# Optimization experiments

Measured on AMD Instinct MI355X. Metric: run time of the kernel, lower is better.

## Reference

```python
import jax, jax.numpy as jnp
import numpy as np

TAU = 0.5

def setup_inputs() -> dict:
    key = jax.random.key(0)
    ks = jax.random.split(key, 20)
    B, D1, D2, E1, E2, U = 4096, 2000, 2000, 256, 256, 512
    M = E1 + E2
    s = lambda k, shp, scale=0.05: jax.random.normal(k, shp, dtype=jnp.float32) * scale
    return {
        "inputs": jax.random.normal(ks[0], (B, D1 + D2), dtype=jnp.float32),
        "h_tm1": jax.random.normal(ks[1], (B, U), dtype=jnp.float32),
        "crohis_tm": jax.random.normal(ks[2], (B, M), dtype=jnp.float32),
        "embed_weight_1": s(ks[3], (D1, E1)),
        "embed_weight_2": s(ks[4], (D2, E2)),
        "ca_1to2_w": s(ks[5], (E1, E1)),
        "ca_1to2_u": s(ks[6], (E2, E1)),
        "ca_1to2_v": s(ks[7], (E2, E1)),
        "ca_2to1_w": s(ks[8], (E2, E2)),
        "ca_2to1_u": s(ks[9], (E1, E2)),
        "ca_2to1_v": s(ks[10], (E1, E2)),
        "crohis_weight_w": s(ks[11], (M, U)),
        "crohis_bias": jnp.zeros((U,), jnp.float32),
        "crohis_decomp_weight": s(ks[12], (M, M)),
        "crohis_decomp_bias": jnp.zeros((M,), jnp.float32),
        "kernel": s(ks[13], (M, 3 * U)),
        "recurrent_kernel": s(ks[14], (U, 3 * U)),
        "bias": jnp.zeros((3 * U,), jnp.float32),
    }


def reference(inputs, h_tm1, crohis_tm,
              embed_weight_1, embed_weight_2,
              ca_1to2_w, ca_1to2_u, ca_1to2_v,
              ca_2to1_w, ca_2to1_u, ca_2to1_v,
              crohis_weight_w, crohis_bias,
              crohis_decomp_weight, crohis_decomp_bias,
              kernel, recurrent_kernel, bias):
    D1 = embed_weight_1.shape[0]
    U = recurrent_kernel.shape[0]
    # dual embedding lookups (dense multi-hot x embedding matrix)
    seqx1 = inputs[:, :D1]
    seqx2 = inputs[:, D1:]
    emb1 = seqx1 @ embed_weight_1   # [B, E1]
    emb2 = seqx2 @ embed_weight_2   # [B, E2]
    # cross-attention gates (softmax over feature axis, as K.softmax default)
    att12 = jax.nn.softmax(jnp.tanh(emb1 @ ca_1to2_w + emb2 @ ca_1to2_u) * (emb2 @ ca_1to2_v), axis=-1)
    att21 = jax.nn.softmax(jnp.tanh(emb2 @ ca_2to1_w + emb1 @ ca_2to1_u) * (emb1 @ ca_2to1_v), axis=-1)
    x = jnp.concatenate([emb1 * att12, emb2 * att21], axis=-1)  # [B, M]
    # cross-history decomposition modulating previous hidden state
    cro = jnp.tanh(crohis_tm @ crohis_decomp_weight + crohis_decomp_bias)
    h_prev = h_tm1 + jnp.tanh(cro @ crohis_weight_w + crohis_bias)
    # GRU (implementation=2, reset_after=False)
    mx = x @ kernel + bias                         # [B, 3U]
    x_z, x_r, x_h = mx[:, :U], mx[:, U:2 * U], mx[:, 2 * U:]
    mi = h_prev @ recurrent_kernel[:, :2 * U]      # [B, 2U]
    z = jax.nn.sigmoid(x_z + mi[:, :U])
    r = jax.nn.sigmoid(x_r + mi[:, U:])
    hh = jnp.tanh(x_h + (r * h_prev) @ recurrent_kernel[:, 2 * U:])
    h = z * h_prev + (1.0 - z) * hh
    # updated cross-history state (exponential moving average with tau)
    crohis_new = TAU * crohis_tm + (1.0 - TAU) * x
    return h, crohis_new
```

## Files before the change

### kernel.cpp

```cpp
#include <hip/hip_runtime.h>
#include <hip/hip_bf16.h>
#include <math.h>


#define TAU_F 0.5f

typedef __bf16 bf16x8 __attribute__((ext_vector_type(8)));
typedef __bf16 bf16x4 __attribute__((ext_vector_type(4)));
typedef float f32x4 __attribute__((ext_vector_type(4)));

__device__ __forceinline__ void gload16(const void* g, void* l) {
    __builtin_amdgcn_global_load_lds(
        (const __attribute__((address_space(1))) void*)g,
        (__attribute__((address_space(3))) void*)l, 16, 0, 0);
}

struct SubGemm {
    const void* A;
    int lda;
    int Kvalid;
    const __bf16* BT;
    int ldbt;
    float* C;
    int ldc;
    long long strideC;
    int Ksub;
    int nbx;
    int pairSplit;
    int pairAOff;
};

template <bool AFP32>
__global__ __launch_bounds__(256) void gemm_dual(SubGemm g1, SubGemm g2, int blocks1)
{
    __shared__ __bf16 As[4][64][32];
    __shared__ __bf16 Bs[4][128][32];

    const int tid = threadIdx.x, w = tid >> 6, l = tid & 63;

    const int gx = gridDim.x;
    const int nwg = gx * (int)gridDim.y;
    const int hw = (int)blockIdx.y * gx + (int)blockIdx.x;
    const int lg = (hw & 7) * (nwg >> 3) + (hw >> 3);
    const int bxl_lin = lg % gx;
    const int by = lg / gx;

    const bool second = bxl_lin >= blocks1;
    const SubGemm& g = second ? g2 : g1;
    const int bxl = second ? bxl_lin - blocks1 : bxl_lin;
    const int ct = bxl % g.nbx, spl = bxl / g.nbx;
    const int brow = by * 64, bcol = ct * 128;
    const int k_begin = spl * g.Ksub;
    const int nt = g.Ksub >> 5;
    float* C = g.C + (size_t)spl * g.strideC;
    const int aoff = (ct >= g.pairSplit) ? g.pairAOff : 0;

    const int sar = w * 16 + (l >> 2);
    const int sbr = w * 32 + (l >> 2);
    const int seg = (l & 3) * 8;

    const __bf16* Ab  = (const __bf16*)g.A + aoff + (size_t)(brow + sar) * g.lda + seg + k_begin;
    const float*  Af  = (const float*)g.A + aoff + (size_t)(brow + sar) * g.lda;
    const __bf16* Bg0 = g.BT + (size_t)(bcol + sbr) * g.ldbt + seg + k_begin;
    const __bf16* Bg1 = Bg0 + (size_t)16 * g.ldbt;
    const int kcl = g.Kvalid - 8;

    f32x4 acc[2][4] = {};
    const int fr = l & 15, fk = (l >> 4) * 8;
    const int wr = (w >> 1) * 32, wc = (w & 1) * 64;
    const int kmax = (nt - 1) * 32;

#define ISSUE_B(slot)                                                      \
    {                                                                      \
        const int _s = (slot);                                             \
        const int _k = (_s * 32 < kmax) ? _s * 32 : kmax;                  \
        const int _b = _s & 3;                                             \
        gload16(Bg0 + _k, &Bs[_b][w * 32][0]);                             \
        gload16(Bg1 + _k, &Bs[_b][w * 32 + 16][0]);                        \
    }
#define ISSUE_AB(slot)                                                     \
    {                                                                      \
        const int _s = (slot);                                             \
        const int _k = (_s * 32 < kmax) ? _s * 32 : kmax;                  \
        const int _b = _s & 3;                                             \
        gload16(Ab + _k,  &As[_b][w * 16][0]);                             \
        gload16(Bg0 + _k, &Bs[_b][w * 32][0]);                             \
        gload16(Bg1 + _k, &Bs[_b][w * 32 + 16][0]);                        \
    }

    if constexpr (AFP32) {
        f32x4 r0a, r0b, r1a, r1b, r2a, r2b, r3a, r3b;

        auto aload = [&](int slot, f32x4& ra, f32x4& rb) {
            int c = k_begin + slot * 32 + seg;
            c = c < kcl ? c : kcl;
            ra = *(const f32x4*)(Af + c);
            rb = *(const f32x4*)(Af + c + 4);
        };
        auto awrite = [&](int bufi, f32x4& ra, f32x4& rb) {
            __bf16 o[8];
#pragma unroll
            for (int z = 0; z < 4; ++z) { o[z] = (__bf16)ra[z]; o[4 + z] = (__bf16)rb[z]; }
            *(bf16x8*)&As[bufi][sar][seg] = *(bf16x8*)o;
        };
        auto astep = [&](int t, f32x4& wa, f32x4& wb, f32x4& la, f32x4& lb) {
            asm volatile("s_waitcnt vmcnt(4)" ::: "memory");
            asm volatile("s_waitcnt lgkmcnt(0)" ::: "memory");
            __builtin_amdgcn_s_barrier();
            const int bi = t & 3;
            bf16x8 a[2], b[4];
#pragma unroll
            for (int m = 0; m < 2; ++m) a[m] = *(const bf16x8*)&As[bi][wr + m * 16 + fr][fk];
#pragma unroll
            for (int n = 0; n < 4; ++n) b[n] = *(const bf16x8*)&Bs[bi][wc + n * 16 + fr][fk];
            awrite((t + 1) & 3, wa, wb);
            aload(t + 3, la, lb);
            ISSUE_B(t + 2)
#pragma unroll
            for (int m = 0; m < 2; ++m)
#pragma unroll
                for (int n = 0; n < 4; ++n)
                    acc[m][n] = __builtin_amdgcn_mfma_f32_16x16x32_bf16(a[m], b[n], acc[m][n], 0, 0, 0);
        };

        aload(0, r0a, r0b);
        asm volatile("s_waitcnt vmcnt(0)" ::: "memory");
        awrite(0, r0a, r0b);
        aload(1, r1a, r1b);
        ISSUE_B(0)
        aload(2, r2a, r2b);
        ISSUE_B(1)

        for (int t = 0; t < nt; t += 4) {
            astep(t,     r1a, r1b, r3a, r3b);
            astep(t + 1, r2a, r2b, r0a, r0b);
            astep(t + 2, r3a, r3b, r1a, r1b);
            astep(t + 3, r0a, r0b, r2a, r2b);
        }
    } else {
        ISSUE_AB(0) ISSUE_AB(1) ISSUE_AB(2)
        for (int t = 0; t < nt; ++t) {
            asm volatile("s_waitcnt vmcnt(6)" ::: "memory");
            asm volatile("s_waitcnt lgkmcnt(0)" ::: "memory");
            __builtin_amdgcn_s_barrier();
            const int bi = t & 3;
            bf16x8 a[2], b[4];
#pragma unroll
            for (int m = 0; m < 2; ++m) a[m] = *(const bf16x8*)&As[bi][wr + m * 16 + fr][fk];
#pragma unroll
            for (int n = 0; n < 4; ++n) b[n] = *(const bf16x8*)&Bs[bi][wc + n * 16 + fr][fk];
            ISSUE_AB(t + 3)
#pragma unroll
            for (int m = 0; m < 2; ++m)
#pragma unroll
                for (int n = 0; n < 4; ++n)
                    acc[m][n] = __builtin_amdgcn_mfma_f32_16x16x32_bf16(a[m], b[n], acc[m][n], 0, 0, 0);
        }
    }
#undef ISSUE_B
#undef ISSUE_AB

    const int fq = (l >> 4) * 4;
#pragma unroll
    for (int m = 0; m < 2; ++m)
#pragma unroll
        for (int n = 0; n < 4; ++n)
#pragma unroll
            for (int r = 0; r < 4; ++r) {
                int row = brow + wr + m * 16 + fq + r;
                int col = bcol + wc + n * 16 + fr;
                C[(size_t)row * g.ldc + col] = acc[m][n][r];
            }
}

__global__ __launch_bounds__(256) void prep_wT(
    const float* __restrict__ ew1, const float* __restrict__ ew2,
    const float* __restrict__ w12, const float* __restrict__ u12,
    const float* __restrict__ v12, const float* __restrict__ w21,
    const float* __restrict__ u21, const float* __restrict__ v21,
    const float* __restrict__ cd_w, const float* __restrict__ cw_w,
    const float* __restrict__ kern, const float* __restrict__ rkern,
    __bf16* __restrict__ WT, __bf16* __restrict__ WcatT,
    __bf16* __restrict__ cdT, __bf16* __restrict__ cwT,
    __bf16* __restrict__ kernT, __bf16* __restrict__ rkernT)
{
    __shared__ float tile[64][65];
    const int b = blockIdx.x, tid = threadIdx.x;
    const int tr = tid >> 6, tc = tid & 63;

    const float* src = nullptr;
    int ldsrc = 0, srow0 = 0, scol0 = 0, kvalid = 1 << 30;
    __bf16* dst; int ldd, n0, k0;
    bool zero = false;

    if (b < 256) {
        int q = b; n0 = (q >> 5) * 64; k0 = (q & 31) * 64;
        dst = WT; ldd = 2048; kvalid = 2000; ldsrc = 256; srow0 = k0;
        if (n0 < 256) { src = ew1; scol0 = n0; } else { src = ew2; scol0 = n0 - 256; }
    } else if (b < 384) {
        int q = b - 256; n0 = (q >> 3) * 64; k0 = (q & 7) * 64;
        dst = WcatT; ldd = 512; ldsrc = 256; srow0 = k0 & 255; scol0 = n0 & 255;
        int qn = n0 >> 8; bool khi = k0 >= 256;
        if (qn == 0)      src = khi ? u12 : w12;
        else if (qn == 1) src = khi ? w21 : u21;
        else if (qn == 2) { if (khi) src = v12; else zero = true; }
        else              { if (khi) zero = true; else src = v21; }
    } else if (b < 448) {
        int q = b - 384; n0 = (q >> 3) * 64; k0 = (q & 7) * 64;
        src = cd_w; ldsrc = 512; srow0 = k0; scol0 = n0; dst = cdT; ldd = 512;
    } else if (b < 512) {
        int q = b - 448; n0 = (q >> 3) * 64; k0 = (q & 7) * 64;
        src = cw_w; ldsrc = 512; srow0 = k0; scol0 = n0; dst = cwT; ldd = 512;
    } else if (b < 704) {
        int q = b - 512; n0 = (q >> 3) * 64; k0 = (q & 7) * 64;
        src = kern; ldsrc = 1536; srow0 = k0; scol0 = n0; dst = kernT; ldd = 512;
    } else {
        int q = b - 704; n0 = (q >> 3) * 64; k0 = (q & 7) * 64;
        src = rkern; ldsrc = 1536; srow0 = k0; scol0 = n0; dst = rkernT; ldd = 512;
    }

#pragma unroll
    for (int p = 0; p < 16; ++p) {
        int kr = p * 4 + tr;
        float v = 0.f;
        if (!zero && (srow0 + kr) < kvalid)
            v = src[(size_t)(srow0 + kr) * ldsrc + scol0 + tc];
        tile[kr][tc] = v;
    }
    __syncthreads();
#pragma unroll
    for (int p = 0; p < 16; ++p) {
        int nr = p * 4 + tr;
        dst[(size_t)(n0 + nr) * ldd + k0 + tc] = (__bf16)tile[tc][nr];
    }
}

__global__ __launch_bounds__(256) void reduce_A(
    const float* __restrict__ P12, const float* __restrict__ P4,
    const float* __restrict__ cd_b,
    __bf16* __restrict__ E, __bf16* __restrict__ cro)
{
    int b = blockIdx.x;
    int i = (((b & 2047) * 256) + threadIdx.x) * 4;
    if (b < 2048) {
        f32x4 p0 = *(const f32x4*)(P12 + i);
        f32x4 p1 = *(const f32x4*)(P12 + (1 << 21) + i);
        __bf16 o[4];
#pragma unroll
        for (int j = 0; j < 4; ++j) o[j] = (__bf16)(p0[j] + p1[j]);
        *(bf16x4*)&E[i] = *(bf16x4*)o;
    } else {
        f32x4 p0 = *(const f32x4*)(P4 + i);
        int c = i & 511;
        __bf16 o[4];
#pragma unroll
        for (int j = 0; j < 4; ++j) o[j] = (__bf16)tanhf(p0[j] + cd_b[c + j]);
        *(bf16x4*)&cro[i] = *(bf16x4*)o;
    }
}

__global__ __launch_bounds__(256) void fuse1(
    const float* __restrict__ T, const __bf16* __restrict__ E,
    const float* __restrict__ crohis,
    const float* __restrict__ P5,
    const float* __restrict__ h_tm1, const float* __restrict__ cw_b,
    __bf16* __restrict__ x, float* __restrict__ cro_out,
    float* __restrict__ hprev, __bf16* __restrict__ hprev_bf)
{
    __shared__ float s4[4];
    int b = blockIdx.x;
    int j = threadIdx.x;
    if (b < 4096) {
        const float* t = T + (size_t)b * 1024;
        float s12 = tanhf(t[j])       * t[512 + j];
        float s21 = tanhf(t[256 + j]) * t[768 + j];
        float v = s12;
#pragma unroll
        for (int o = 32; o >= 1; o >>= 1) v = fmaxf(v, __shfl_xor(v, o, 64));
        __syncthreads(); if ((j & 63) == 0) s4[j >> 6] = v; __syncthreads();
        float m12 = fmaxf(fmaxf(s4[0], s4[1]), fmaxf(s4[2], s4[3]));
        float e12 = expf(s12 - m12);
        v = e12;
#pragma unroll
        for (int o = 32; o >= 1; o >>= 1) v += __shfl_xor(v, o, 64);
        __syncthreads(); if ((j & 63) == 0) s4[j >> 6] = v; __syncthreads();
        float sum12 = s4[0] + s4[1] + s4[2] + s4[3];
        v = s21;
#pragma unroll
        for (int o = 32; o >= 1; o >>= 1) v = fmaxf(v, __shfl_xor(v, o, 64));
        __syncthreads(); if ((j & 63) == 0) s4[j >> 6] = v; __syncthreads();
        float m21 = fmaxf(fmaxf(s4[0], s4[1]), fmaxf(s4[2], s4[3]));
        float e21 = expf(s21 - m21);
        v = e21;
#pragma unroll
        for (int o = 32; o >= 1; o >>= 1) v += __shfl_xor(v, o, 64);
        __syncthreads(); if ((j & 63) == 0) s4[j >> 6] = v; __syncthreads();
        float sum21 = s4[0] + s4[1] + s4[2] + s4[3];

        size_t b0 = (size_t)b * 512 + j, b1 = b0 + 256;
        float x1 = (float)E[b0] * (e12 / sum12);
        float x2 = (float)E[b1] * (e21 / sum21);
        x[b0] = (__bf16)x1;
        x[b1] = (__bf16)x2;
        cro_out[b0] = TAU_F * crohis[b0] + (1.f - TAU_F) * x1;
        cro_out[b1] = TAU_F * crohis[b1] + (1.f - TAU_F) * x2;
    } else {
        int i = ((b - 4096) * 256 + j) * 4;
        f32x4 p = *(const f32x4*)(P5 + i);
        f32x4 ht = *(const f32x4*)(h_tm1 + i);
        int c = i & 511;
        f32x4 o; __bf16 ob[4];
#pragma unroll
        for (int q = 0; q < 4; ++q) {
            float hv = ht[q] + tanhf(p[q] + cw_b[c + q]);
            o[q] = hv; ob[q] = (__bf16)hv;
        }
        *(f32x4*)(hprev + i) = o;
        *(bf16x4*)&hprev_bf[i] = *(bf16x4*)ob;
    }
}

__global__ __launch_bounds__(256) void gates_k(
    const float* __restrict__ mx, const float* __restrict__ mi2,
    const float* __restrict__ hprev, const float* __restrict__ bias,
    __bf16* __restrict__ rh)
{
    int i = (blockIdx.x * 256 + threadIdx.x) * 4;
    int row = i >> 9, c = i & 511;
    f32x4 a  = *(const f32x4*)(mx + (size_t)row * 1536 + 512 + c);
    f32x4 m  = *(const f32x4*)(mi2 + (size_t)row * 1024 + 512 + c);
    f32x4 hp = *(const f32x4*)(hprev + i);
    f32x4 bb = *(const f32x4*)(bias + 512 + c);
    __bf16 o[4];
#pragma unroll
    for (int q = 0; q < 4; ++q) {
        float r = 1.f / (1.f + expf(-(a[q] + bb[q] + m[q])));
        o[q] = (__bf16)(r * hp[q]);
    }
    *(bf16x4*)&rh[i] = *(bf16x4*)o;
}

__global__ __launch_bounds__(256) void final_k(
    const float* __restrict__ mx, const float* __restrict__ mi2,
    const float* __restrict__ P8a, const float* __restrict__ P8b,
    const float* __restrict__ hprev, const float* __restrict__ bias,
    float* __restrict__ h)
{
    int i = (blockIdx.x * 256 + threadIdx.x) * 4;
    int row = i >> 9, c = i & 511;
    f32x4 xz = *(const f32x4*)(mx + (size_t)row * 1536 + c);
    f32x4 xh = *(const f32x4*)(mx + (size_t)row * 1536 + 1024 + c);
    f32x4 mz = *(const f32x4*)(mi2 + (size_t)row * 1024 + c);
    f32x4 p0 = *(const f32x4*)(P8a + i);
    f32x4 p1 = *(const f32x4*)(P8b + i);
    f32x4 hp = *(const f32x4*)(hprev + i);
    f32x4 bz = *(const f32x4*)(bias + c);
    f32x4 bh = *(const f32x4*)(bias + 1024 + c);
    f32x4 o;
#pragma unroll
    for (int q = 0; q < 4; ++q) {
        float z = 1.f / (1.f + expf(-(xz[q] + bz[q] + mz[q])));
        float hh = tanhf(xh[q] + bh[q] + p0[q] + p1[q]);
        o[q] = z * hp[q] + (1.f - z) * hh;
    }
    *(f32x4*)(h + i) = o;
}

extern "C" void kernel_launch(void* const* d_in, const int* in_sizes, int n_in,
                              void* d_out, int out_size, void* d_ws, size_t ws_size,
                              hipStream_t stream)
{
    (void)in_sizes; (void)n_in; (void)out_size; (void)ws_size;

    const float* inputs = (const float*)d_in[0];
    const float* h_tm1  = (const float*)d_in[1];
    const float* crohis = (const float*)d_in[2];
    const float* ew1    = (const float*)d_in[3];
    const float* ew2    = (const float*)d_in[4];
    const float* ca12w  = (const float*)d_in[5];
    const float* ca12u  = (const float*)d_in[6];
    const float* ca12v  = (const float*)d_in[7];
    const float* ca21w  = (const float*)d_in[8];
    const float* ca21u  = (const float*)d_in[9];
    const float* ca21v  = (const float*)d_in[10];
    const float* cw_w   = (const float*)d_in[11];
    const float* cw_b   = (const float*)d_in[12];
    const float* cd_w   = (const float*)d_in[13];
    const float* cd_b   = (const float*)d_in[14];
    const float* kern   = (const float*)d_in[15];
    const float* rkern  = (const float*)d_in[16];
    const float* bias   = (const float*)d_in[17];

    char* ws = (char*)d_ws;
    const size_t MB = 1 << 20;
    float*  P12      = (float*)(ws + 0);
    float*  P4       = (float*)(ws + 16 * MB);
    __bf16* E        = (__bf16*)(ws + 32 * MB);
    __bf16* cro_bf   = (__bf16*)(ws + 36 * MB);
    float*  T        = (float*)(ws + 0);
    float*  P5       = (float*)(ws + 16 * MB);
    __bf16* x        = (__bf16*)(ws + 40 * MB);
    float*  hprev    = (float*)(ws + 24 * MB);
    __bf16* hprev_bf = (__bf16*)(ws + 64 * MB);
    float*  mx       = (float*)(ws + 0);
    float*  mi2      = (float*)(ws + 44 * MB);
    __bf16* rh       = (__bf16*)(ws + 32 * MB);
    float*  P8       = (float*)(ws + 36 * MB);
    float*  P8b      = (float*)(ws + 60 * MB);
    __bf16* WT       = (__bf16*)(ws + 68 * MB);
    __bf16* WcatT    = (__bf16*)(ws + 70 * MB);
    __bf16* cdT      = (__bf16*)(ws + 71 * MB);
    __bf16* cwT      = (__bf16*)(ws + 71 * MB + 512 * 1024);
    __bf16* kernT    = (__bf16*)(ws + 72 * MB);
    __bf16* rkernT   = (__bf16*)(ws + 73 * MB + 512 * 1024);

    float* h_out   = (float*)d_out;
    float* cro_out = (float*)d_out + 2 * 1048576;

    const int BIG = 1 << 30;

    prep_wT<<<896, 256, 0, stream>>>(ew1, ew2, ca12w, ca12u, ca12v, ca21w,
                                     ca21u, ca21v, cd_w, cw_w, kern, rkern,
                                     WT, WcatT, cdT, cwT, kernT, rkernT);

    SubGemm gA1 = { inputs, 4000, 2000, WT,  2048, P12, 512, 1ll << 21, 1024, 4, 2, 2000 };
    SubGemm gA2 = { crohis,  512,  512, cdT,  512, P4,  512, 0,          512, 4, BIG, 0 };
    gemm_dual<true><<<dim3(12, 64), 256, 0, stream>>>(gA1, gA2, 8);

    reduce_A<<<4096, 256, 0, stream>>>(P12, P4, cd_b, E, cro_bf);

    SubGemm gB1 = { E,      512, 512, WcatT, 512, T,  1024, 0, 512, 8, BIG, 0 };
    SubGemm gB2 = { cro_bf, 512, 512, cwT,   512, P5, 512,  0, 512, 4, BIG, 0 };
    gemm_dual<false><<<dim3(12, 64), 256, 0, stream>>>(gB1, gB2, 8);

    fuse1<<<6144, 256, 0, stream>>>(T, E, crohis, P5, h_tm1, cw_b,
                                    x, cro_out, hprev, hprev_bf);

    SubGemm gC1 = { x,        512, 512, kernT,  512, mx,  1536, 0, 512, 12, BIG, 0 };
    SubGemm gC2 = { hprev_bf, 512, 512, rkernT, 512, mi2, 1024, 0, 512, 8,  BIG, 0 };
    gemm_dual<false><<<dim3(20, 64), 256, 0, stream>>>(gC1, gC2, 12);

    gates_k<<<2048, 256, 0, stream>>>(mx, mi2, hprev, bias, rh);

    SubGemm gG = { rh, 512, 512, rkernT + (size_t)1024 * 512, 512, P8, 512, 6ll << 20, 256, 4, BIG, 0 };
    gemm_dual<false><<<dim3(8, 64), 256, 0, stream>>>(gG, gG, 8);

    final_k<<<2048, 256, 0, stream>>>(mx, mi2, P8, P8b, hprev, bias, h_out);
}
```

Measured before the change: 134.5 us.

## Switch GEMMs to 128x128 single-buffered tiles with more split-K partials

The GEMM kernel drops its 4-stage software pipeline with async global-to-LDS loads and moves to a simple single-buffered loop with __syncthreads, while growing the block tile from 64x128 to 128x128 (4x4 MFMAs per wave). To keep enough blocks in flight, the first two GEMM stages use more split-K slices, and the reduce and fuse kernels now sum the extra partial buffers. The workspace layout is reshuffled to fit the added partials. Larger tiles raise reuse per block, but losing the pipelining exposes memory latency and the extra partials add more traffic.

After: 137.7 us. +2.4%, slower.

```diff
diff --git a/kernel.cpp b/kernel.cpp
--- a/kernel.cpp
+++ b/kernel.cpp
@@ -33,8 +33,8 @@
 template <bool AFP32>
 __global__ __launch_bounds__(256) void gemm_dual(SubGemm g1, SubGemm g2, int blocks1)
 {
-    __shared__ __bf16 As[4][64][32];
-    __shared__ __bf16 Bs[4][128][32];
+    __shared__ __bf16 As[128][32];
+    __shared__ __bf16 Bs[128][32];
 
     const int tid = threadIdx.x, w = tid >> 6, l = tid & 63;
 
@@ -49,120 +49,69 @@
     const SubGemm& g = second ? g2 : g1;
     const int bxl = second ? bxl_lin - blocks1 : bxl_lin;
     const int ct = bxl % g.nbx, spl = bxl / g.nbx;
-    const int brow = by * 64, bcol = ct * 128;
+    const int brow = by * 128, bcol = ct * 128;
     const int k_begin = spl * g.Ksub;
     const int nt = g.Ksub >> 5;
     float* C = g.C + (size_t)spl * g.strideC;
     const int aoff = (ct >= g.pairSplit) ? g.pairAOff : 0;
 
-    const int sar = w * 16 + (l >> 2);
-    const int sbr = w * 32 + (l >> 2);
+    const int sr  = w * 32 + (l >> 2);
     const int seg = (l & 3) * 8;
 
-    const __bf16* Ab  = (const __bf16*)g.A + aoff + (size_t)(brow + sar) * g.lda + seg + k_begin;
-    const float*  Af  = (const float*)g.A + aoff + (size_t)(brow + sar) * g.lda;
-    const __bf16* Bg0 = g.BT + (size_t)(bcol + sbr) * g.ldbt + seg + k_begin;
+    const __bf16* Ab0 = (const __bf16*)g.A + aoff + (size_t)(brow + sr) * g.lda + seg + k_begin;
+    const __bf16* Ab1 = Ab0 + (size_t)16 * g.lda;
+    const float*  Af0 = (const float*)g.A + aoff + (size_t)(brow + sr) * g.lda;
+    const float*  Af1 = Af0 + (size_t)16 * g.lda;
+    const __bf16* Bg0 = g.BT + (size_t)(bcol + sr) * g.ldbt + seg + k_begin;
     const __bf16* Bg1 = Bg0 + (size_t)16 * g.ldbt;
     const int kcl = g.Kvalid - 8;
 
-    f32x4 acc[2][4] = {};
+    f32x4 acc[4][4] = {};
     const int fr = l & 15, fk = (l >> 4) * 8;
-    const int wr = (w >> 1) * 32, wc = (w & 1) * 64;
-    const int kmax = (nt - 1) * 32;
-
-#define ISSUE_B(slot)                                                      \
-    {                                                                      \
-        const int _s = (slot);                                             \
-        const int _k = (_s * 32 < kmax) ? _s * 32 : kmax;                  \
-        const int _b = _s & 3;                                             \
-        gload16(Bg0 + _k, &Bs[_b][w * 32][0]);                             \
-        gload16(Bg1 + _k, &Bs[_b][w * 32 + 16][0]);                        \
-    }
-#define ISSUE_AB(slot)                                                     \
-    {                                                                      \
-        const int _s = (slot);                                             \
-        const int _k = (_s * 32 < kmax) ? _s * 32 : kmax;                  \
-        const int _b = _s & 3;                                             \
-        gload16(Ab + _k,  &As[_b][w * 16][0]);                             \
-        gload16(Bg0 + _k, &Bs[_b][w * 32][0]);                             \
-        gload16(Bg1 + _k, &Bs[_b][w * 32 + 16][0]);                        \
-    }
-
-    if constexpr (AFP32) {
-        f32x4 r0a, r0b, r1a, r1b, r2a, r2b, r3a, r3b;
-
-        auto aload = [&](int slot, f32x4& ra, f32x4& rb) {
-            int c = k_begin + slot * 32 + seg;
+    const int wr = (w >> 1) * 64, wc = (w & 1) * 64;
+
+    for (int t = 0; t < nt; ++t) {
+        const int k = t * 32;
+        __syncthreads();
+        if constexpr (AFP32) {
+            int c = k_begin + k + seg;
             c = c < kcl ? c : kcl;
-            ra = *(const f32x4*)(Af + c);
-            rb = *(const f32x4*)(Af + c + 4);
-        };
-        auto awrite = [&](int bufi, f32x4& ra, f32x4& rb) {
+            f32x4 v0 = *(const f32x4*)(Af0 + c);
+            f32x4 v1 = *(const f32x4*)(Af0 + c + 4);
+            f32x4 v2 = *(const f32x4*)(Af1 + c);
+            f32x4 v3 = *(const f32x4*)(Af1 + c + 4);
+            gload16(Bg0 + k, &Bs[w * 32][0]);
+            gload16(Bg1 + k, &Bs[w * 32 + 16][0]);
             __bf16 o[8];
 #pragma unroll
-            for (int z = 0; z < 4; ++z) { o[z] = (__bf16)ra[z]; o[4 + z] = (__bf16)rb[z]; }
-            *(bf16x8*)&As[bufi][sar][seg] = *(bf16x8*)o;
-        };
-        auto astep = [&](int t, f32x4& wa, f32x4& wb, f32x4& la, f32x4& lb) {
-            asm volatile("s_waitcnt vmcnt(4)" ::: "memory");
-            asm volatile("s_waitcnt lgkmcnt(0)" ::: "memory");
-            __builtin_amdgcn_s_barrier();
-            const int bi = t & 3;
-            bf16x8 a[2], b[4];
-#pragma unroll
-            for (int m = 0; m < 2; ++m) a[m] = *(const bf16x8*)&As[bi][wr + m * 16 + fr][fk];
-#pragma unroll
-            for (int n = 0; n < 4; ++n) b[n] = *(const bf16x8*)&Bs[bi][wc + n * 16 + fr][fk];
-            awrite((t + 1) & 3, wa, wb);
-            aload(t + 3, la, lb);
-            ISSUE_B(t + 2)
-#pragma unroll
-            for (int m = 0; m < 2; ++m)
-#pragma unroll
-                for (int n = 0; n < 4; ++n)
-                    acc[m][n] = __builtin_amdgcn_mfma_f32_16x16x32_bf16(a[m], b[n], acc[m][n], 0, 0, 0);
-        };
-
-        aload(0, r0a, r0b);
-        asm volatile("s_waitcnt vmcnt(0)" ::: "memory");
-        awrite(0, r0a, r0b);
-        aload(1, r1a, r1b);
-        ISSUE_B(0)
-        aload(2, r2a, r2b);
-        ISSUE_B(1)
-
-        for (int t = 0; t < nt; t += 4) {
-            astep(t,     r1a, r1b, r3a, r3b);
-            astep(t + 1, r2a, r2b, r0a, r0b);
-            astep(t + 2, r3a, r3b, r1a, r1b);
-            astep(t + 3, r0a, r0b, r2a, r2b);
+            for (int z = 0; z < 4; ++z) { o[z] = (__bf16)v0[z]; o[4 + z] = (__bf16)v1[z]; }
+            *(bf16x8*)&As[sr][seg] = *(bf16x8*)o;
+#pragma unroll
+            for (int z = 0; z < 4; ++z) { o[z] = (__bf16)v2[z]; o[4 + z] = (__bf16)v3[z]; }
+            *(bf16x8*)&As[sr + 16][seg] = *(bf16x8*)o;
+        } else {
+            gload16(Ab0 + k, &As[w * 32][0]);
+            gload16(Ab1 + k, &As[w * 32 + 16][0]);
+            gload16(Bg0 + k, &Bs[w * 32][0]);
+            gload16(Bg1 + k, &Bs[w * 32 + 16][0]);
         }
-    } else {
-        ISSUE_AB(0) ISSUE_AB(1) ISSUE_AB(2)
-        for (int t = 0; t < nt; ++t) {
-            asm volatile("s_waitcnt vmcnt(6)" ::: "memory");
-            asm volatile("s_waitcnt lgkmcnt(0)" ::: "memory");
-            __builtin_amdgcn_s_barrier();
-            const int bi = t & 3;
-            bf16x8 a[2], b[4];
-#pragma unroll
-            for (int m = 0; m < 2; ++m) a[m] = *(const bf16x8*)&As[bi][wr + m * 16 + fr][fk];
-#pragma unroll
-            for (int n = 0; n < 4; ++n) b[n] = *(const bf16x8*)&Bs[bi][wc + n * 16 + fr][fk];
-            ISSUE_AB(t + 3)
-#pragma unroll
-            for (int m = 0; m < 2; ++m)
-#pragma unroll
-                for (int n = 0; n < 4; ++n)
-                    acc[m][n] = __builtin_amdgcn_mfma_f32_16x16x32_bf16(a[m], b[n], acc[m][n], 0, 0, 0);
-        }
-    }
-#undef ISSUE_B
-#undef ISSUE_AB
+        __syncthreads();
+
+        bf16x8 a[4], b[4];
+#pragma unroll
+        for (int m = 0; m < 4; ++m) a[m] = *(const bf16x8*)&As[wr + m * 16 + fr][fk];
+#pragma unroll
+        for (int n = 0; n < 4; ++n) b[n] = *(const bf16x8*)&Bs[wc + n * 16 + fr][fk];
+#pragma unroll
+        for (int m = 0; m < 4; ++m)
+#pragma unroll
+            for (int n = 0; n < 4; ++n)
+                acc[m][n] = __builtin_amdgcn_mfma_f32_16x16x32_bf16(a[m], b[n], acc[m][n], 0, 0, 0);
+    }
 
     const int fq = (l >> 4) * 4;
 #pragma unroll
-    for (int m = 0; m < 2; ++m)
+    for (int m = 0; m < 4; ++m)
 #pragma unroll
         for (int n = 0; n < 4; ++n)
 #pragma unroll
@@ -240,29 +189,33 @@
     const float* __restrict__ cd_b,
     __bf16* __restrict__ E, __bf16* __restrict__ cro)
 {
+    const int S = 1 << 21;
     int b = blockIdx.x;
     int i = (((b & 2047) * 256) + threadIdx.x) * 4;
     if (b < 2048) {
         f32x4 p0 = *(const f32x4*)(P12 + i);
-        f32x4 p1 = *(const f32x4*)(P12 + (1 << 21) + i);
+        f32x4 p1 = *(const f32x4*)(P12 + S + i);
+        f32x4 p2 = *(const f32x4*)(P12 + 2 * S + i);
+        f32x4 p3 = *(const f32x4*)(P12 + 3 * S + i);
         __bf16 o[4];
 #pragma unroll
-        for (int j = 0; j < 4; ++j) o[j] = (__bf16)(p0[j] + p1[j]);
+        for (int j = 0; j < 4; ++j) o[j] = (__bf16)(p0[j] + p1[j] + p2[j] + p3[j]);
         *(bf16x4*)&E[i] = *(bf16x4*)o;
     } else {
         f32x4 p0 = *(const f32x4*)(P4 + i);
+        f32x4 p1 = *(const f32x4*)(P4 + S + i);
         int c = i & 511;
         __bf16 o[4];
 #pragma unroll
-        for (int j = 0; j < 4; ++j) o[j] = (__bf16)tanhf(p0[j] + cd_b[c + j]);
+        for (int j = 0; j < 4; ++j) o[j] = (__bf16)tanhf(p0[j] + p1[j] + cd_b[c + j]);
         *(bf16x4*)&cro[i] = *(bf16x4*)o;
     }
 }
 
 __global__ __launch_bounds__(256) void fuse1(
-    const float* __restrict__ T, const __bf16* __restrict__ E,
-    const float* __restrict__ crohis,
-    const float* __restrict__ P5,
+    const float* __restrict__ P3a, const float* __restrict__ P3b,
+    const __bf16* __restrict__ E, const float* __restrict__ crohis,
+    const float* __restrict__ P5a, const float* __restrict__ P5b,
     const float* __restrict__ h_tm1, const float* __restrict__ cw_b,
     __bf16* __restrict__ x, float* __restrict__ cro_out,
     float* __restrict__ hprev, __bf16* __restrict__ hprev_bf)
@@ -271,9 +224,13 @@
     int b = blockIdx.x;
     int j = threadIdx.x;
     if (b < 4096) {
-        const float* t = T + (size_t)b * 1024;
-        float s12 = tanhf(t[j])       * t[512 + j];
-        float s21 = tanhf(t[256 + j]) * t[768 + j];
+        size_t base = (size_t)b * 1024;
+        float t0 = P3a[base + j]       + P3b[base + j];
+        float t1 = P3a[base + 256 + j] + P3b[base + 256 + j];
+        float t2 = P3a[base + 512 + j] + P3b[base + 512 + j];
+        float t3 = P3a[base + 768 + j] + P3b[base + 768 + j];
+        float s12 = tanhf(t0) * t2;
+        float s21 = tanhf(t1) * t3;
         float v = s12;
 #pragma unroll
         for (int o = 32; o >= 1; o >>= 1) v = fmaxf(v, __shfl_xor(v, o, 64));
@@ -306,13 +263,14 @@
         cro_out[b1] = TAU_F * crohis[b1] + (1.f - TAU_F) * x2;
     } else {
         int i = ((b - 4096) * 256 + j) * 4;
-        f32x4 p = *(const f32x4*)(P5 + i);
+        f32x4 p0 = *(const f32x4*)(P5a + i);
+        f32x4 p1 = *(const f32x4*)(P5b + i);
         f32x4 ht = *(const f32x4*)(h_tm1 + i);
         int c = i & 511;
         f32x4 o; __bf16 ob[4];
 #pragma unroll
         for (int q = 0; q < 4; ++q) {
-            float hv = ht[q] + tanhf(p[q] + cw_b[c + q]);
+            float hv = ht[q] + tanhf(p0[q] + p1[q] + cw_b[c + q]);
             o[q] = hv; ob[q] = (__bf16)hv;
         }
         *(f32x4*)(hprev + i) = o;
@@ -394,19 +352,18 @@
     char* ws = (char*)d_ws;
     const size_t MB = 1 << 20;
     float*  P12      = (float*)(ws + 0);
-    float*  P4       = (float*)(ws + 16 * MB);
-    __bf16* E        = (__bf16*)(ws + 32 * MB);
-    __bf16* cro_bf   = (__bf16*)(ws + 36 * MB);
-    float*  T        = (float*)(ws + 0);
-    float*  P5       = (float*)(ws + 16 * MB);
-    __bf16* x        = (__bf16*)(ws + 40 * MB);
-    float*  hprev    = (float*)(ws + 24 * MB);
-    __bf16* hprev_bf = (__bf16*)(ws + 64 * MB);
+    float*  P4       = (float*)(ws + 32 * MB);
+    __bf16* E        = (__bf16*)(ws + 48 * MB);
+    __bf16* cro_bf   = (__bf16*)(ws + 52 * MB);
+    float*  P3       = (float*)(ws + 0);
+    float*  P5       = (float*)(ws + 32 * MB);
+    __bf16* x        = (__bf16*)(ws + 56 * MB);
+    float*  hprev    = (float*)(ws + 60 * MB);
+    __bf16* hprev_bf = (__bf16*)(ws + 52 * MB);
     float*  mx       = (float*)(ws + 0);
-    float*  mi2      = (float*)(ws + 44 * MB);
-    __bf16* rh       = (__bf16*)(ws + 32 * MB);
-    float*  P8       = (float*)(ws + 36 * MB);
-    float*  P8b      = (float*)(ws + 60 * MB);
+    float*  mi2      = (float*)(ws + 24 * MB);
+    __bf16* rh       = (__bf16*)(ws + 40 * MB);
+    float*  P8       = (float*)(ws + 44 * MB);
     __bf16* WT       = (__bf16*)(ws + 68 * MB);
     __bf16* WcatT    = (__bf16*)(ws + 70 * MB);
     __bf16* cdT      = (__bf16*)(ws + 71 * MB);
@@ -418,32 +375,34 @@
     float* cro_out = (float*)d_out + 2 * 1048576;
 
     const int BIG = 1 << 30;
+    const long long S2 = 1ll << 21;
+    const long long S4 = 1ll << 22;
 
     prep_wT<<<896, 256, 0, stream>>>(ew1, ew2, ca12w, ca12u, ca12v, ca21w,
                                      ca21u, ca21v, cd_w, cw_w, kern, rkern,
                                      WT, WcatT, cdT, cwT, kernT, rkernT);
 
-    SubGemm gA1 = { inputs, 4000, 2000, WT,  2048, P12, 512, 1ll << 21, 1024, 4, 2, 2000 };
-    SubGemm gA2 = { crohis,  512,  512, cdT,  512, P4,  512, 0,          512, 4, BIG, 0 };
-    gemm_dual<true><<<dim3(12, 64), 256, 0, stream>>>(gA1, gA2, 8);
+    SubGemm gA1 = { inputs, 4000, 2000, WT,  2048, P12, 512, S2, 512, 4, 2, 2000 };
+    SubGemm gA2 = { crohis,  512,  512, cdT,  512, P4,  512, S2, 256, 4, BIG, 0 };
+    gemm_dual<true><<<dim3(24, 32), 256, 0, stream>>>(gA1, gA2, 16);
 
     reduce_A<<<4096, 256, 0, stream>>>(P12, P4, cd_b, E, cro_bf);
 
-    SubGemm gB1 = { E,      512, 512, WcatT, 512, T,  1024, 0, 512, 8, BIG, 0 };
-    SubGemm gB2 = { cro_bf, 512, 512, cwT,   512, P5, 512,  0, 512, 4, BIG, 0 };
-    gemm_dual<false><<<dim3(12, 64), 256, 0, stream>>>(gB1, gB2, 8);
-
-    fuse1<<<6144, 256, 0, stream>>>(T, E, crohis, P5, h_tm1, cw_b,
-                                    x, cro_out, hprev, hprev_bf);
+    SubGemm gB1 = { E,      512, 512, WcatT, 512, P3, 1024, S4, 256, 8, BIG, 0 };
+    SubGemm gB2 = { cro_bf, 512, 512, cwT,   512, P5, 512,  S2, 256, 4, BIG, 0 };
+    gemm_dual<false><<<dim3(24, 32), 256, 0, stream>>>(gB1, gB2, 16);
+
+    fuse1<<<6144, 256, 0, stream>>>(P3, P3 + S4, E, crohis, P5, P5 + S2,
+                                    h_tm1, cw_b, x, cro_out, hprev, hprev_bf);
 
     SubGemm gC1 = { x,        512, 512, kernT,  512, mx,  1536, 0, 512, 12, BIG, 0 };
     SubGemm gC2 = { hprev_bf, 512, 512, rkernT, 512, mi2, 1024, 0, 512, 8,  BIG, 0 };
-    gemm_dual<false><<<dim3(20, 64), 256, 0, stream>>>(gC1, gC2, 12);
+    gemm_dual<false><<<dim3(20, 32), 256, 0, stream>>>(gC1, gC2, 12);
 
     gates_k<<<2048, 256, 0, stream>>>(mx, mi2, hprev, bias, rh);
 
-    SubGemm gG = { rh, 512, 512, rkernT + (size_t)1024 * 512, 512, P8, 512, 6ll << 20, 256, 4, BIG, 0 };
-    gemm_dual<false><<<dim3(8, 64), 256, 0, stream>>>(gG, gG, 8);
-
-    final_k<<<2048, 256, 0, stream>>>(mx, mi2, P8, P8b, hprev, bias, h_out);
-}
+    SubGemm gG = { rh, 512, 512, rkernT + (size_t)1024 * 512, 512, P8, 512, S2, 256, 4, BIG, 0 };
+    gemm_dual<false><<<dim3(8, 32), 256, 0, stream>>>(gG, gG, 8);
+
+    final_k<<<2048, 256, 0, stream>>>(mx, mi2, P8, P8 + S2, hprev, bias, h_out);
+}
```

## Stream fp32 A tiles directly to LDS, emit bf16 attention output, repack workspace

Applied to the files above, without the earlier changes.

The fp32-A GEMM path now loads fp32 tiles straight into LDS with async global_load_lds through a 3-stage buffer and converts them to bf16 when reading from LDS. This replaces the register-staged load, convert and LDS-write pipeline. The attention-logit GEMM (T) now writes bf16 instead of fp32, which halves its store and the later fuse1 read. The workspace layout is reorganised to match. The trade-offs are less precision in T, double the LDS traffic for A in the first GEMM, and one fewer pipeline stage.

Result: no change. 132.7 us (-1.3%).

```diff
diff --git a/kernel.cpp b/kernel.cpp
--- a/kernel.cpp
+++ b/kernel.cpp
@@ -28,13 +28,13 @@
     int nbx;
     int pairSplit;
     int pairAOff;
+    int obf16;
 };
 
 template <bool AFP32>
 __global__ __launch_bounds__(256) void gemm_dual(SubGemm g1, SubGemm g2, int blocks1)
 {
-    __shared__ __bf16 As[4][64][32];
-    __shared__ __bf16 Bs[4][128][32];
+    __shared__ __attribute__((aligned(16))) char lds[49152];
 
     const int tid = threadIdx.x, w = tid >> 6, l = tid & 63;
 
@@ -52,125 +52,138 @@
     const int brow = by * 64, bcol = ct * 128;
     const int k_begin = spl * g.Ksub;
     const int nt = g.Ksub >> 5;
-    float* C = g.C + (size_t)spl * g.strideC;
     const int aoff = (ct >= g.pairSplit) ? g.pairAOff : 0;
 
-    const int sar = w * 16 + (l >> 2);
     const int sbr = w * 32 + (l >> 2);
     const int seg = (l & 3) * 8;
 
-    const __bf16* Ab  = (const __bf16*)g.A + aoff + (size_t)(brow + sar) * g.lda + seg + k_begin;
-    const float*  Af  = (const float*)g.A + aoff + (size_t)(brow + sar) * g.lda;
     const __bf16* Bg0 = g.BT + (size_t)(bcol + sbr) * g.ldbt + seg + k_begin;
     const __bf16* Bg1 = Bg0 + (size_t)16 * g.ldbt;
-    const int kcl = g.Kvalid - 8;
 
     f32x4 acc[2][4] = {};
     const int fr = l & 15, fk = (l >> 4) * 8;
     const int wr = (w >> 1) * 32, wc = (w & 1) * 64;
     const int kmax = (nt - 1) * 32;
 
-#define ISSUE_B(slot)                                                      \
-    {                                                                      \
-        const int _s = (slot);                                             \
-        const int _k = (_s * 32 < kmax) ? _s * 32 : kmax;                  \
-        const int _b = _s & 3;                                             \
-        gload16(Bg0 + _k, &Bs[_b][w * 32][0]);                             \
-        gload16(Bg1 + _k, &Bs[_b][w * 32 + 16][0]);                        \
-    }
-#define ISSUE_AB(slot)                                                     \
-    {                                                                      \
-        const int _s = (slot);                                             \
-        const int _k = (_s * 32 < kmax) ? _s * 32 : kmax;                  \
-        const int _b = _s & 3;                                             \
-        gload16(Ab + _k,  &As[_b][w * 16][0]);                             \
-        gload16(Bg0 + _k, &Bs[_b][w * 32][0]);                             \
-        gload16(Bg1 + _k, &Bs[_b][w * 32 + 16][0]);                        \
-    }
-
     if constexpr (AFP32) {
-        f32x4 r0a, r0b, r1a, r1b, r2a, r2b, r3a, r3b;
-
-        auto aload = [&](int slot, f32x4& ra, f32x4& rb) {
-            int c = k_begin + slot * 32 + seg;
-            c = c < kcl ? c : kcl;
-            ra = *(const f32x4*)(Af + c);
-            rb = *(const f32x4*)(Af + c + 4);
-        };
-        auto awrite = [&](int bufi, f32x4& ra, f32x4& rb) {
-            __bf16 o[8];
-#pragma unroll
-            for (int z = 0; z < 4; ++z) { o[z] = (__bf16)ra[z]; o[4 + z] = (__bf16)rb[z]; }
-            *(bf16x8*)&As[bufi][sar][seg] = *(bf16x8*)o;
-        };
-        auto astep = [&](int t, f32x4& wa, f32x4& wb, f32x4& la, f32x4& lb) {
+        auto Af32 = (float (*)[64][32])lds;
+        auto Bs   = (__bf16 (*)[128][32])(lds + 24576);
+
+        const float* ArowBase = (const float*)g.A + aoff
+                              + (size_t)(brow + w * 16 + (l >> 3)) * g.lda;
+        const int colLane = (l & 7) * 4;
+        const int kcl4 = g.Kvalid - 4;
+
+#define ISSUE_A32(slot)                                                       \
+        {                                                                     \
+            const int _s = (slot);                                            \
+            const int _k = (_s * 32 < kmax) ? _s * 32 : kmax;                 \
+            const int _b = _s % 3;                                            \
+            int c0 = k_begin + _k + colLane;                                  \
+            c0 = c0 < kcl4 ? c0 : kcl4;                                       \
+            gload16(ArowBase + c0,                 &Af32[_b][w * 16][0]);     \
+            gload16(ArowBase + 8 * g.lda + c0,     &Af32[_b][w * 16 + 8][0]); \
+            gload16(Bg0 + _k, &Bs[_b][w * 32][0]);                            \
+            gload16(Bg1 + _k, &Bs[_b][w * 32 + 16][0]);                       \
+        }
+
+        ISSUE_A32(0) ISSUE_A32(1)
+
+        for (int t = 0; t < nt; ++t) {
             asm volatile("s_waitcnt vmcnt(4)" ::: "memory");
             asm volatile("s_waitcnt lgkmcnt(0)" ::: "memory");
             __builtin_amdgcn_s_barrier();
-            const int bi = t & 3;
-            bf16x8 a[2], b[4];
-#pragma unroll
-            for (int m = 0; m < 2; ++m) a[m] = *(const bf16x8*)&As[bi][wr + m * 16 + fr][fk];
+
+            const int bi = t % 3;
+            bf16x8 a[2]; bf16x8 b[4];
+#pragma unroll
+            for (int m = 0; m < 2; ++m) {
+                f32x4 lo = *(const f32x4*)&Af32[bi][wr + m * 16 + fr][fk];
+                f32x4 hi = *(const f32x4*)&Af32[bi][wr + m * 16 + fr][fk + 4];
+#pragma unroll
+                for (int z = 0; z < 4; ++z) { a[m][z] = (__bf16)lo[z]; a[m][4 + z] = (__bf16)hi[z]; }
+            }
 #pragma unroll
             for (int n = 0; n < 4; ++n) b[n] = *(const bf16x8*)&Bs[bi][wc + n * 16 + fr][fk];
-            awrite((t + 1) & 3, wa, wb);
-            aload(t + 3, la, lb);
-            ISSUE_B(t + 2)
+
+            ISSUE_A32(t + 2)
+
 #pragma unroll
             for (int m = 0; m < 2; ++m)
 #pragma unroll
                 for (int n = 0; n < 4; ++n)
                     acc[m][n] = __builtin_amdgcn_mfma_f32_16x16x32_bf16(a[m], b[n], acc[m][n], 0, 0, 0);
-        };
-
-        aload(0, r0a, r0b);
-        asm volatile("s_waitcnt vmcnt(0)" ::: "memory");
-        awrite(0, r0a, r0b);
-        aload(1, r1a, r1b);
-        ISSUE_B(0)
-        aload(2, r2a, r2b);
-        ISSUE_B(1)
-
-        for (int t = 0; t < nt; t += 4) {
-            astep(t,     r1a, r1b, r3a, r3b);
-            astep(t + 1, r2a, r2b, r0a, r0b);
-            astep(t + 2, r3a, r3b, r1a, r1b);
-            astep(t + 3, r0a, r0b, r2a, r2b);
         }
+#undef ISSUE_A32
     } else {
+        auto As = (__bf16 (*)[64][32])lds;
+        auto Bs = (__bf16 (*)[128][32])(lds + 16384);
+
+        const int sar = w * 16 + (l >> 2);
+        const __bf16* Ar = (const __bf16*)g.A + aoff
+                         + (size_t)(brow + sar) * g.lda + seg + k_begin;
+
+#define ISSUE_AB(slot)                                                        \
+        {                                                                     \
+            const int _s = (slot);                                            \
+            const int _k = (_s * 32 < kmax) ? _s * 32 : kmax;                 \
+            const int _b = _s & 3;                                            \
+            gload16(Ar + _k,  &As[_b][w * 16][0]);                            \
+            gload16(Bg0 + _k, &Bs[_b][w * 32][0]);                            \
+            gload16(Bg1 + _k, &Bs[_b][w * 32 + 16][0]);                       \
+        }
+
         ISSUE_AB(0) ISSUE_AB(1) ISSUE_AB(2)
+
         for (int t = 0; t < nt; ++t) {
             asm volatile("s_waitcnt vmcnt(6)" ::: "memory");
             asm volatile("s_waitcnt lgkmcnt(0)" ::: "memory");
             __builtin_amdgcn_s_barrier();
+
             const int bi = t & 3;
             bf16x8 a[2], b[4];
 #pragma unroll
             for (int m = 0; m < 2; ++m) a[m] = *(const bf16x8*)&As[bi][wr + m * 16 + fr][fk];
 #pragma unroll
             for (int n = 0; n < 4; ++n) b[n] = *(const bf16x8*)&Bs[bi][wc + n * 16 + fr][fk];
+
             ISSUE_AB(t + 3)
+
 #pragma unroll
             for (int m = 0; m < 2; ++m)
 #pragma unroll
                 for (int n = 0; n < 4; ++n)
                     acc[m][n] = __builtin_amdgcn_mfma_f32_16x16x32_bf16(a[m], b[n], acc[m][n], 0, 0, 0);
         }
-    }
-#undef ISSUE_B
 #undef ISSUE_AB
+    }
 
     const int fq = (l >> 4) * 4;
-#pragma unroll
-    for (int m = 0; m < 2; ++m)
-#pragma unroll
-        for (int n = 0; n < 4; ++n)
-#pragma unroll
-            for (int r = 0; r < 4; ++r) {
-                int row = brow + wr + m * 16 + fq + r;
-                int col = bcol + wc + n * 16 + fr;
-                C[(size_t)row * g.ldc + col] = acc[m][n][r];
-            }
+    if (g.obf16) {
+        __bf16* Cb = (__bf16*)g.C + (size_t)spl * g.strideC;
+#pragma unroll
+        for (int m = 0; m < 2; ++m)
+#pragma unroll
+            for (int n = 0; n < 4; ++n)
+#pragma unroll
+                for (int r = 0; r < 4; ++r) {
+                    int row = brow + wr + m * 16 + fq + r;
+                    int col = bcol + wc + n * 16 + fr;
+                    Cb[(size_t)row * g.ldc + col] = (__bf16)acc[m][n][r];
+                }
+    } else {
+        float* C = g.C + (size_t)spl * g.strideC;
+#pragma unroll
+        for (int m = 0; m < 2; ++m)
+#pragma unroll
+            for (int n = 0; n < 4; ++n)
+#pragma unroll
+                for (int r = 0; r < 4; ++r) {
+                    int row = brow + wr + m * 16 + fq + r;
+                    int col = bcol + wc + n * 16 + fr;
+                    C[(size_t)row * g.ldc + col] = acc[m][n][r];
+                }
+    }
 }
 
 __global__ __launch_bounds__(256) void prep_wT(
@@ -240,11 +253,12 @@
     const float* __restrict__ cd_b,
     __bf16* __restrict__ E, __bf16* __restrict__ cro)
 {
+    const int S = 1 << 21;
     int b = blockIdx.x;
     int i = (((b & 2047) * 256) + threadIdx.x) * 4;
     if (b < 2048) {
         f32x4 p0 = *(const f32x4*)(P12 + i);
-        f32x4 p1 = *(const f32x4*)(P12 + (1 << 21) + i);
+        f32x4 p1 = *(const f32x4*)(P12 + S + i);
         __bf16 o[4];
 #pragma unroll
         for (int j = 0; j < 4; ++j) o[j] = (__bf16)(p0[j] + p1[j]);
@@ -260,7 +274,7 @@
 }
 
 __global__ __launch_bounds__(256) void fuse1(
-    const float* __restrict__ T, const __bf16* __restrict__ E,
+    const __bf16* __restrict__ T, const __bf16* __restrict__ E,
     const float* __restrict__ crohis,
     const float* __restrict__ P5,
     const float* __restrict__ h_tm1, const float* __restrict__ cw_b,
@@ -271,9 +285,9 @@
     int b = blockIdx.x;
     int j = threadIdx.x;
     if (b < 4096) {
-        const float* t = T + (size_t)b * 1024;
-        float s12 = tanhf(t[j])       * t[512 + j];
-        float s21 = tanhf(t[256 + j]) * t[768 + j];
+        const __bf16* t = T + (size_t)b * 1024;
+        float s12 = tanhf((float)t[j])       * (float)t[512 + j];
+        float s21 = tanhf((float)t[256 + j]) * (float)t[768 + j];
         float v = s12;
 #pragma unroll
         for (int o = 32; o >= 1; o >>= 1) v = fmaxf(v, __shfl_xor(v, o, 64));
@@ -395,55 +409,55 @@
     const size_t MB = 1 << 20;
     float*  P12      = (float*)(ws + 0);
     float*  P4       = (float*)(ws + 16 * MB);
-    __bf16* E        = (__bf16*)(ws + 32 * MB);
-    __bf16* cro_bf   = (__bf16*)(ws + 36 * MB);
-    float*  T        = (float*)(ws + 0);
-    float*  P5       = (float*)(ws + 16 * MB);
+    __bf16* T        = (__bf16*)(ws + 16 * MB);
+    float*  P5       = (float*)(ws + 32 * MB);
     __bf16* x        = (__bf16*)(ws + 40 * MB);
-    float*  hprev    = (float*)(ws + 24 * MB);
-    __bf16* hprev_bf = (__bf16*)(ws + 64 * MB);
+    __bf16* rh       = (__bf16*)(ws + 40 * MB);
+    float*  P8       = (float*)(ws + 44 * MB);
+    __bf16* E        = (__bf16*)(ws + 48 * MB);
+    __bf16* cro_bf   = (__bf16*)(ws + 52 * MB);
+    float*  hprev    = (float*)(ws + 60 * MB);
+    __bf16* hprev_bf = (__bf16*)(ws + 68 * MB);
     float*  mx       = (float*)(ws + 0);
-    float*  mi2      = (float*)(ws + 44 * MB);
-    __bf16* rh       = (__bf16*)(ws + 32 * MB);
-    float*  P8       = (float*)(ws + 36 * MB);
-    float*  P8b      = (float*)(ws + 60 * MB);
-    __bf16* WT       = (__bf16*)(ws + 68 * MB);
-    __bf16* WcatT    = (__bf16*)(ws + 70 * MB);
-    __bf16* cdT      = (__bf16*)(ws + 71 * MB);
-    __bf16* cwT      = (__bf16*)(ws + 71 * MB + 512 * 1024);
-    __bf16* kernT    = (__bf16*)(ws + 72 * MB);
-    __bf16* rkernT   = (__bf16*)(ws + 73 * MB + 512 * 1024);
+    float*  mi2      = (float*)(ws + 24 * MB);
+    __bf16* WT       = (__bf16*)(ws + 72 * MB);
+    __bf16* WcatT    = (__bf16*)(ws + 74 * MB);
+    __bf16* cdT      = (__bf16*)(ws + 75 * MB);
+    __bf16* cwT      = (__bf16*)(ws + 75 * MB + 512 * 1024);
+    __bf16* kernT    = (__bf16*)(ws + 76 * MB);
+    __bf16* rkernT   = (__bf16*)(ws + 77 * MB + 512 * 1024);
 
     float* h_out   = (float*)d_out;
     float* cro_out = (float*)d_out + 2 * 1048576;
 
     const int BIG = 1 << 30;
+    const long long S2 = 1ll << 21;
 
     prep_wT<<<896, 256, 0, stream>>>(ew1, ew2, ca12w, ca12u, ca12v, ca21w,
                                      ca21u, ca21v, cd_w, cw_w, kern, rkern,
                                      WT, WcatT, cdT, cwT, kernT, rkernT);
 
-    SubGemm gA1 = { inputs, 4000, 2000, WT,  2048, P12, 512, 1ll << 21, 1024, 4, 2, 2000 };
-    SubGemm gA2 = { crohis,  512,  512, cdT,  512, P4,  512, 0,          512, 4, BIG, 0 };
+    SubGemm gA1 = { inputs, 4000, 2000, WT,  2048, P12, 512, S2, 1024, 4, 2, 2000, 0 };
+    SubGemm gA2 = { crohis,  512,  512, cdT,  512, P4,  512, 0,   512, 4, BIG, 0, 0 };
     gemm_dual<true><<<dim3(12, 64), 256, 0, stream>>>(gA1, gA2, 8);
 
     reduce_A<<<4096, 256, 0, stream>>>(P12, P4, cd_b, E, cro_bf);
 
-    SubGemm gB1 = { E,      512, 512, WcatT, 512, T,  1024, 0, 512, 8, BIG, 0 };
-    SubGemm gB2 = { cro_bf, 512, 512, cwT,   512, P5, 512,  0, 512, 4, BIG, 0 };
+    SubGemm gB1 = { E,      512, 512, WcatT, 512, (float*)T, 1024, 0, 512, 8, BIG, 0, 1 };
+    SubGemm gB2 = { cro_bf, 512, 512, cwT,   512, P5,        512,  0, 512, 4, BIG, 0, 0 };
     gemm_dual<false><<<dim3(12, 64), 256, 0, stream>>>(gB1, gB2, 8);
 
     fuse1<<<6144, 256, 0, stream>>>(T, E, crohis, P5, h_tm1, cw_b,
                                     x, cro_out, hprev, hprev_bf);
 
-    SubGemm gC1 = { x,        512, 512, kernT,  512, mx,  1536, 0, 512, 12, BIG, 0 };
-    SubGemm gC2 = { hprev_bf, 512, 512, rkernT, 512, mi2, 1024, 0, 512, 8,  BIG, 0 };
+    SubGemm gC1 = { x,        512, 512, kernT,  512, mx,  1536, 0, 512, 12, BIG, 0, 0 };
+    SubGemm gC2 = { hprev_bf, 512, 512, rkernT, 512, mi2, 1024, 0, 512, 8,  BIG, 0, 0 };
     gemm_dual<false><<<dim3(20, 64), 256, 0, stream>>>(gC1, gC2, 12);
 
     gates_k<<<2048, 256, 0, stream>>>(mx, mi2, hprev, bias, rh);
 
-    SubGemm gG = { rh, 512, 512, rkernT + (size_t)1024 * 512, 512, P8, 512, 6ll << 20, 256, 4, BIG, 0 };
+    SubGemm gG = { rh, 512, 512, rkernT + (size_t)1024 * 512, 512, P8, 512, S2, 256, 4, BIG, 0, 0 };
     gemm_dual<false><<<dim3(8, 64), 256, 0, stream>>>(gG, gG, 8);
 
-    final_k<<<2048, 256, 0, stream>>>(mx, mi2, P8, P8b, hprev, bias, h_out);
-}
+    final_k<<<2048, 256, 0, stream>>>(mx, mi2, P8, P8 + S2, hprev, bias, h_out);
+}
```
